# Kernel tuning notes

Hardware: AMD Instinct MI355X
Metric: run time of the kernel (lower is better)

Reference implementation:

```python
import jax, jax.numpy as jnp
import numpy as np

B, L, D, H = 4, 2048, 1024, 16
HD = D // H  # head_dim = 64


def setup_inputs() -> dict:
    key = jax.random.key(0)
    k1, k2, k3 = jax.random.split(key, 3)
    scale_in = 1.0 / np.sqrt(D)
    return {
        "x": jax.random.normal(k1, (B, L, D), dtype=jnp.float32),
        "Wqkv": jax.random.normal(k2, (D, 3 * D), dtype=jnp.float32) * scale_in,
        "Wout": jax.random.normal(k3, (D, D), dtype=jnp.float32) * scale_in,
        "bout": jnp.zeros((D,), dtype=jnp.float32),
    }


def reference(x, Wqkv, Wout, bout):
    b, l, d = x.shape
    # QKV projection (no bias): [B, L, 3D] -> [B, L, 3, H, HD]
    qkv = (x @ Wqkv).reshape(b, l, 3, H, HD)
    q, k, v = jnp.moveaxis(qkv, 2, 0)  # each [B, L, H, HD]
    # scaled scores [B, H, L, L]
    scores = jnp.einsum("blhd,bmhd->bhlm", q, k) / jnp.sqrt(jnp.float32(HD))
    causal_mask = jnp.triu(jnp.ones((l, l), dtype=bool), k=1)
    scores = jnp.where(causal_mask, -jnp.inf, scores)
    attn = jax.nn.softmax(scores, axis=-1)
    # dropout p=0.0 (eval-mode reference) -> identity
    out = jnp.einsum("bhlm,bmhd->blhd", attn, v).reshape(b, l, d)
    return out @ Wout + bout
```

## Files before the change

### kernel.cpp

```cpp
#include <hip/hip_runtime.h>

typedef unsigned short ushort_t;
using bf16x8 = __attribute__((ext_vector_type(8))) short;
using f32x4  = __attribute__((ext_vector_type(4))) float;
using f32x16 = __attribute__((ext_vector_type(16))) float;
using u32x4  = __attribute__((ext_vector_type(4))) unsigned int;

#define B_  4
#define L_  2048
#define D_  1024
#define H_  16
#define HD_ 64
#define N3_ 3072
#define M1_ (B_ * L_)

static __device__ __forceinline__ unsigned short f2bf(float f) {
    unsigned int u = __float_as_uint(f);
    unsigned int r = (u + 0x7fffu + ((u >> 16) & 1u)) >> 16;
    return (unsigned short)r;
}

static __device__ __forceinline__ unsigned int pkbf(float lo, float hi) {
    unsigned int r;
    asm("v_cvt_pk_bf16_f32 %0, %1, %2" : "=v"(r) : "v"(lo), "v"(hi));
    return r;
}

static __device__ __forceinline__ void plswap(unsigned int& a, unsigned int& b) {
    asm volatile("v_permlane32_swap_b32 %0, %1" : "+v"(a), "+v"(b));
}

static __device__ __forceinline__ void async16(const void* g, const void* l) {
    __builtin_amdgcn_global_load_lds(
        (const __attribute__((address_space(1))) void*)g,
        (__attribute__((address_space(3))) void*)l, 16, 0, 0);
}

__global__ void convert_x_kernel(const float4* __restrict__ src,
                                 ushort4* __restrict__ dst) {
    int i = blockIdx.x * blockDim.x + threadIdx.x;
    float4 v = src[i];
    ushort4 o;
    o.x = f2bf(v.x); o.y = f2bf(v.y); o.z = f2bf(v.z); o.w = f2bf(v.w);
    dst[i] = o;
}

__global__ void transpose_conv_kernel(const float* __restrict__ src,
                                      unsigned short* __restrict__ dst,
                                      int rows, int cols) {
    __shared__ float tile[32][33];
    int tx = threadIdx.x, ty = threadIdx.y;
    int c0 = blockIdx.x * 32, r0 = blockIdx.y * 32;
    #pragma unroll
    for (int j = 0; j < 32; j += 8)
        tile[ty + j][tx] = src[(size_t)(r0 + ty + j) * cols + c0 + tx];
    __syncthreads();
    #pragma unroll
    for (int j = 0; j < 32; j += 8)
        dst[(size_t)(c0 + ty + j) * rows + r0 + tx] = f2bf(tile[tx][ty + j]);
}

__global__ __launch_bounds__(512, 4) void gemm256_qkv_kernel(
    const unsigned short* __restrict__ A, const unsigned short* __restrict__ BT,
    unsigned short* __restrict__ qb, unsigned short* __restrict__ kb,
    unsigned short* __restrict__ vb) {
    constexpr int K = 1024, BK = 32, NT = K / BK;
    constexpr int NBX = N3_ / 128;
    constexpr int NWG = (M1_ / 256) * NBX;
    __shared__ __align__(16) unsigned short ldsA[3][256 * BK];
    __shared__ __align__(16) unsigned short ldsB[3][128 * BK];

    const int tid = threadIdx.x;
    const int w = tid >> 6, lane = tid & 63;
    const int wr = w >> 2, wc = w & 3;
    const int lg = lane >> 4, ll = lane & 15;

    const int bid = blockIdx.x;
    const int swz = (bid & 7) * (NWG / 8) + (bid >> 3);
    const int m0 = (swz / NBX) * 256, n0 = (swz % NBX) * 128;

    const int srow = tid >> 2;
    const int scol = (((tid & 3) ^ ((tid >> 3) & 3)) * 8);
    const int rxor = ((ll >> 1) & 3) * 8;

    f32x4 acc[8][2] = {};

    #define STAGE(kt_) do {                                                  \
        const int b3_ = (kt_) % 3;                                           \
        const size_t koff_ = (size_t)(kt_) * BK + scol;                      \
        async16(&A[(size_t)(m0 + srow) * K + koff_],       &ldsA[b3_][tid * 8]);        \
        async16(&A[(size_t)(m0 + 128 + srow) * K + koff_], &ldsA[b3_][4096 + tid * 8]); \
        async16(&BT[(size_t)(n0 + srow) * K + koff_],      &ldsB[b3_][tid * 8]);        \
    } while (0)

    STAGE(0);
    STAGE(1);

    #pragma unroll 1
    for (int kt = 0; kt < NT; ++kt) {
        if (kt + 2 < NT) {
            STAGE(kt + 2);
            asm volatile("s_waitcnt vmcnt(6)" ::: "memory");
        } else if (kt + 1 < NT) {
            asm volatile("s_waitcnt vmcnt(3)" ::: "memory");
        } else {
            asm volatile("s_waitcnt vmcnt(0)" ::: "memory");
        }
        __builtin_amdgcn_s_barrier();
        __builtin_amdgcn_sched_barrier(0);

        const unsigned short* Ab = &ldsA[kt % 3][0];
        const unsigned short* Bb = &ldsB[kt % 3][0];
        bf16x8 bfr[2];
        #pragma unroll
        for (int j = 0; j < 2; ++j)
            bfr[j] = *(const bf16x8*)&Bb[(wc * 32 + j * 16 + ll) * BK + (lg * 8 ^ rxor)];
        bf16x8 af[8];
        #pragma unroll
        for (int i = 0; i < 8; ++i)
            af[i] = *(const bf16x8*)&Ab[(wr * 128 + i * 16 + ll) * BK + (lg * 8 ^ rxor)];

        __builtin_amdgcn_s_setprio(1);
        #pragma unroll
        for (int i = 0; i < 8; ++i)
            #pragma unroll
            for (int j = 0; j < 2; ++j)
                acc[i][j] = __builtin_amdgcn_mfma_f32_16x16x32_bf16(
                    af[i], bfr[j], acc[i][j], 0, 0, 0);
        __builtin_amdgcn_s_setprio(0);
        __builtin_amdgcn_s_barrier();
    }
    #undef STAGE

    #pragma unroll
    for (int mi = 0; mi < 8; ++mi) {
        const int mb = m0 + wr * 128 + mi * 16 + lg * 4;
        #pragma unroll
        for (int ni = 0; ni < 2; ++ni) {
            const int n = n0 + wc * 32 + ni * 16 + ll;
            const int s = n >> 10, h = (n >> 6) & 15, hd = n & 63;
            if (s == 2) {
                const int b = mb >> 11, l = mb & 2047;
                const size_t base = (size_t)(b * H_ + h) * (L_ * HD_);
                ushort4 pk;
                pk.x = f2bf(acc[mi][ni][0]);
                pk.y = f2bf(acc[mi][ni][1]);
                pk.z = f2bf(acc[mi][ni][2]);
                pk.w = f2bf(acc[mi][ni][3]);
                *(ushort4*)&vb[base + (l >> 5) * 2048 + ((l >> 4) & 1) * 1024 +
                               ((l >> 3) & 1) * 512 + hd * 8 + (l & 7)] = pk;
            } else {
                #pragma unroll
                for (int r = 0; r < 4; ++r) {
                    const int m = mb + r;
                    const int b = m >> 11, l = m & 2047;
                    const size_t base = (size_t)(b * H_ + h) * (L_ * HD_);
                    const size_t o = base + (l >> 5) * 2048 + (hd >> 4) * 512 +
                                     ((hd >> 3) & 1) * 256 + (l & 31) * 8 + (hd & 7);
                    unsigned short bv = f2bf(acc[mi][ni][r]);
                    if (s == 0) qb[o] = bv; else kb[o] = bv;
                }
            }
        }
    }
}

__global__ __launch_bounds__(256) void gemm_bt_kernel(
    const unsigned short* __restrict__ A, const unsigned short* __restrict__ BT,
    float* __restrict__ outp, const float* __restrict__ bias) {
    constexpr int K = 1024;
    __shared__ unsigned short As[128 * 32];
    __shared__ unsigned short Bs[128 * 32];
    const int tid = threadIdx.x, w = tid >> 6, lane = tid & 63;
    const int m0 = blockIdx.y * 128, n0 = blockIdx.x * 128;
    const int wm = (w >> 1) * 64, wn = (w & 1) * 64;
    const int lg = lane >> 4, ll = lane & 15;
    const int scol = (((lane & 3) ^ ((lane >> 3) & 3)) * 8);
    const int rxor = ((ll >> 1) & 3) * 8;

    f32x4 acc[4][4] = {};

    for (int k0 = 0; k0 < K; k0 += 32) {
        #pragma unroll
        for (int j = 0; j < 2; ++j) {
            int row = w * 32 + j * 16 + (lane >> 2);
            async16(&A[(size_t)(m0 + row) * K + k0 + scol], &As[(w * 32 + j * 16) * 32]);
            async16(&BT[(size_t)(n0 + row) * K + k0 + scol], &Bs[(w * 32 + j * 16) * 32]);
        }
        __syncthreads();
        bf16x8 af[4], bfr[4];
        #pragma unroll
        for (int i = 0; i < 4; ++i) {
            af[i]  = *(const bf16x8*)&As[(wm + i * 16 + ll) * 32 + (lg * 8 ^ rxor)];
            bfr[i] = *(const bf16x8*)&Bs[(wn + i * 16 + ll) * 32 + (lg * 8 ^ rxor)];
        }
        #pragma unroll
        for (int mi = 0; mi < 4; ++mi)
            #pragma unroll
            for (int ni = 0; ni < 4; ++ni)
                acc[mi][ni] = __builtin_amdgcn_mfma_f32_16x16x32_bf16(
                    af[mi], bfr[ni], acc[mi][ni], 0, 0, 0);
        __syncthreads();
    }

    #pragma unroll
    for (int mi = 0; mi < 4; ++mi)
        #pragma unroll
        for (int ni = 0; ni < 4; ++ni)
            #pragma unroll
            for (int r = 0; r < 4; ++r) {
                int m = m0 + wm + mi * 16 + lg * 4 + r;
                int n = n0 + wn + ni * 16 + ll;
                outp[(size_t)m * D_ + n] = acc[mi][ni][r] + bias[n];
            }
}

__global__ __launch_bounds__(256) void attn_kernel(
    const unsigned short* __restrict__ qbuf, const unsigned short* __restrict__ kbuf,
    const unsigned short* __restrict__ vbuf, unsigned short* __restrict__ obuf) {
    __shared__ __align__(16) unsigned short ldsK[2][2048];
    __shared__ __align__(16) unsigned short ldsV[2][2048];
    __shared__ float Sden[4][32];

    const int tid = threadIdx.x;
    const int w = tid >> 6, lane = tid & 63;
    const int lq = lane & 31;
    const int hi = lane >> 5;

    const int bid = blockIdx.x;
    const int grp = bid >> 6;
    const int bh  = bid & 63;
    const int qt  = (15 - grp) * 4 + w;
    const int q0  = qt * 32;
    const int ntmax = (15 - grp) * 4 + 4;

    const unsigned short* Qf = qbuf + (size_t)bh * (L_ * HD_);
    const unsigned short* Kf = kbuf + (size_t)bh * (L_ * HD_);
    const unsigned short* Vf = vbuf + (size_t)bh * (L_ * HD_);

    bf16x8 qf[4];
    #pragma unroll
    for (int c = 0; c < 4; ++c)
        qf[c] = *(const bf16x8*)&Qf[qt * 2048 + c * 512 + hi * 256 + lq * 8];

    f32x16 oa0 = {}, oa1 = {};
    float sden = 0.f;

    const float C1 = 0.18033688011112042f;
    const float C2 = 7.2134752044448165f;

    async16(&Kf[tid * 8], &ldsK[0][tid * 8]);
    async16(&Vf[tid * 8], &ldsV[0][tid * 8]);

    #pragma unroll 1
    for (int t = 0; t < ntmax; ++t) {
        if (t + 1 < ntmax) {
            async16(&Kf[(size_t)(t + 1) * 2048 + tid * 8], &ldsK[(t + 1) & 1][tid * 8]);
            async16(&Vf[(size_t)(t + 1) * 2048 + tid * 8], &ldsV[(t + 1) & 1][tid * 8]);
            asm volatile("s_waitcnt vmcnt(2)" ::: "memory");
        } else {
            asm volatile("s_waitcnt vmcnt(0)" ::: "memory");
        }
        __builtin_amdgcn_s_barrier();
        __builtin_amdgcn_sched_barrier(0);

        if (t <= qt) {
            const unsigned short* Kb = &ldsK[t & 1][0];
            const unsigned short* Vb = &ldsV[t & 1][0];

            f32x16 st = {};
            __builtin_amdgcn_s_setprio(1);
            #pragma unroll
            for (int c = 0; c < 4; ++c) {
                bf16x8 kf = *(const bf16x8*)&Kb[c * 512 + hi * 256 + lq * 8];
                st = __builtin_amdgcn_mfma_f32_32x32x16_bf16(kf, qf[c], st, 0, 0, 0);
            }
            __builtin_amdgcn_s_setprio(0);

            float p[16];
            float rs = 0.f;
            const bool diag = (t == qt);
            #pragma unroll
            for (int r = 0; r < 16; ++r) {
                float pv = exp2f(fmaf(st[r], C1, -C2));
                if (diag) {
                    int kv = (r & 3) + 8 * (r >> 2) + 4 * hi;
                    if (kv > lq) pv = 0.f;
                }
                p[r] = pv;
                rs += pv;
            }
            rs += __shfl_xor(rs, 32);
            sden += rs;

            unsigned int a0 = pkbf(p[0],  p[1]),  a1 = pkbf(p[2],  p[3]);
            unsigned int b0 = pkbf(p[4],  p[5]),  b1 = pkbf(p[6],  p[7]);
            unsigned int c0 = pkbf(p[8],  p[9]),  c1 = pkbf(p[10], p[11]);
            unsigned int d0 = pkbf(p[12], p[13]), d1 = pkbf(p[14], p[15]);
            plswap(a0, b0);
            plswap(a1, b1);
            plswap(c0, d0);
            plswap(c1, d1);
            u32x4 t0 = {a0, a1, b0, b1};
            u32x4 t1 = {c0, c1, d0, d1};
            bf16x8 pa0 = __builtin_bit_cast(bf16x8, t0);
            bf16x8 pa1 = __builtin_bit_cast(bf16x8, t1);

            __builtin_amdgcn_s_setprio(1);
            #pragma unroll
            for (int c = 0; c < 2; ++c) {
                bf16x8 v0f = *(const bf16x8*)&Vb[c * 1024 + hi * 512 + lq * 8];
                bf16x8 v1f = *(const bf16x8*)&Vb[c * 1024 + hi * 512 + 256 + lq * 8];
                bf16x8 pa = (c == 0) ? pa0 : pa1;
                oa0 = __builtin_amdgcn_mfma_f32_32x32x16_bf16(pa, v0f, oa0, 0, 0, 0);
                oa1 = __builtin_amdgcn_mfma_f32_32x32x16_bf16(pa, v1f, oa1, 0, 0, 0);
            }
            __builtin_amdgcn_s_setprio(0);
        }
        __builtin_amdgcn_s_barrier();
    }

    if (hi == 0) Sden[w][lq] = 1.0f / sden;
    __builtin_amdgcn_s_waitcnt(0);

    const int b = bh >> 4, h = bh & 15;
    #pragma unroll
    for (int r = 0; r < 16; ++r) {
        int q = (r & 3) + 8 * (r >> 2) + 4 * hi;
        float inv = Sden[w][q];
        float o0 = oa0[r] * inv;
        float o1 = oa1[r] * inv;
        size_t row = (size_t)(b * L_ + q0 + q) * D_ + h * HD_;
        obuf[row + lq]      = f2bf(o0);
        obuf[row + 32 + lq] = f2bf(o1);
    }
}

extern "C" void kernel_launch(void* const* d_in, const int* in_sizes, int n_in,
                              void* d_out, int out_size, void* d_ws, size_t ws_size,
                              hipStream_t stream) {
    const float* x    = (const float*)d_in[0];
    const float* Wqkv = (const float*)d_in[1];
    const float* Wout = (const float*)d_in[2];
    const float* bout = (const float*)d_in[3];
    float* out = (float*)d_out;

    char* ws = (char*)d_ws;
    size_t off = 0;
    unsigned short* xb     = (unsigned short*)(ws + off); off += (size_t)M1_ * D_ * 2;
    unsigned short* wqkvT  = (unsigned short*)(ws + off); off += (size_t)N3_ * D_ * 2;
    unsigned short* woutT  = (unsigned short*)(ws + off); off += (size_t)D_ * D_ * 2;
    unsigned short* qb     = (unsigned short*)(ws + off); off += (size_t)B_ * H_ * L_ * HD_ * 2;
    unsigned short* kb     = (unsigned short*)(ws + off); off += (size_t)B_ * H_ * L_ * HD_ * 2;
    unsigned short* vb     = (unsigned short*)(ws + off); off += (size_t)B_ * H_ * L_ * HD_ * 2;
    unsigned short* attnb  = (unsigned short*)(ws + off); off += (size_t)M1_ * D_ * 2;

    convert_x_kernel<<<(M1_ * D_ / 4) / 256, 256, 0, stream>>>(
        (const float4*)x, (ushort4*)xb);
    transpose_conv_kernel<<<dim3(N3_ / 32, D_ / 32), dim3(32, 8), 0, stream>>>(
        Wqkv, wqkvT, D_, N3_);
    transpose_conv_kernel<<<dim3(D_ / 32, D_ / 32), dim3(32, 8), 0, stream>>>(
        Wout, woutT, D_, D_);

    gemm256_qkv_kernel<<<dim3((M1_ / 256) * (N3_ / 128)), 512, 0, stream>>>(
        xb, wqkvT, qb, kb, vb);

    attn_kernel<<<dim3(16 * 64), 256, 0, stream>>>(qb, kb, vb, attnb);

    gemm_bt_kernel<<<dim3(D_ / 128, M1_ / 128), 256, 0, stream>>>(
        attnb, woutT, out, bout);
}
```

Before: 199.1 us.

## Pair complementary causal query tiles per wave and load K/V directly to registers

Each wave now processes two query tiles (qt and 63-qt) so every wave does balanced causal work, sharing each K/V tile load between both. The shared-memory double buffer and block barriers are removed, and K/V fragments are read straight from global memory into registers with a one-tile K prefetch. The grid is halved to 512 blocks. This trades LDS reuse across the four waves for per-wave global loads, and raises register pressure while cutting occupancy.

```diff
diff --git a/kernel.cpp b/kernel.cpp
--- a/kernel.cpp
+++ b/kernel.cpp
@@ -218,9 +218,7 @@
 __global__ __launch_bounds__(256) void attn_kernel(
     const unsigned short* __restrict__ qbuf, const unsigned short* __restrict__ kbuf,
     const unsigned short* __restrict__ vbuf, unsigned short* __restrict__ obuf) {
-    __shared__ __align__(16) unsigned short ldsK[2][2048];
-    __shared__ __align__(16) unsigned short ldsV[2][2048];
-    __shared__ float Sden[4][32];
+    __shared__ float Sden[4][2][32];
 
     const int tid = threadIdx.x;
     const int w = tid >> 6, lane = tid & 63;
@@ -228,111 +226,156 @@
     const int hi = lane >> 5;
 
     const int bid = blockIdx.x;
-    const int grp = bid >> 6;
-    const int bh  = bid & 63;
-    const int qt  = (15 - grp) * 4 + w;
-    const int q0  = qt * 32;
-    const int ntmax = (15 - grp) * 4 + 4;
+    const int g  = bid >> 6;
+    const int bh = bid & 63;
+    const int pa = g * 4 + w;
+    const int qtA = pa, qtB = 63 - pa;
 
     const unsigned short* Qf = qbuf + (size_t)bh * (L_ * HD_);
     const unsigned short* Kf = kbuf + (size_t)bh * (L_ * HD_);
     const unsigned short* Vf = vbuf + (size_t)bh * (L_ * HD_);
 
-    bf16x8 qf[4];
-    #pragma unroll
-    for (int c = 0; c < 4; ++c)
-        qf[c] = *(const bf16x8*)&Qf[qt * 2048 + c * 512 + hi * 256 + lq * 8];
-
-    f32x16 oa0 = {}, oa1 = {};
-    float sden = 0.f;
+    bf16x8 qfA[4], qfB[4];
+    #pragma unroll
+    for (int c = 0; c < 4; ++c) {
+        qfA[c] = *(const bf16x8*)&Qf[qtA * 2048 + c * 512 + hi * 256 + lq * 8];
+        qfB[c] = *(const bf16x8*)&Qf[qtB * 2048 + c * 512 + hi * 256 + lq * 8];
+    }
+
+    f32x16 oaA0 = {}, oaA1 = {}, oaB0 = {}, oaB1 = {};
+    float sdenA = 0.f, sdenB = 0.f;
 
     const float C1 = 0.18033688011112042f;
     const float C2 = 7.2134752044448165f;
 
-    async16(&Kf[tid * 8], &ldsK[0][tid * 8]);
-    async16(&Vf[tid * 8], &ldsV[0][tid * 8]);
+    bf16x8 kf[4];
+    #pragma unroll
+    for (int c = 0; c < 4; ++c)
+        kf[c] = *(const bf16x8*)&Kf[c * 512 + hi * 256 + lq * 8];
 
     #pragma unroll 1
-    for (int t = 0; t < ntmax; ++t) {
-        if (t + 1 < ntmax) {
-            async16(&Kf[(size_t)(t + 1) * 2048 + tid * 8], &ldsK[(t + 1) & 1][tid * 8]);
-            async16(&Vf[(size_t)(t + 1) * 2048 + tid * 8], &ldsV[(t + 1) & 1][tid * 8]);
-            asm volatile("s_waitcnt vmcnt(2)" ::: "memory");
-        } else {
-            asm volatile("s_waitcnt vmcnt(0)" ::: "memory");
-        }
-        __builtin_amdgcn_s_barrier();
-        __builtin_amdgcn_sched_barrier(0);
-
-        if (t <= qt) {
-            const unsigned short* Kb = &ldsK[t & 1][0];
-            const unsigned short* Vb = &ldsV[t & 1][0];
-
-            f32x16 st = {};
-            __builtin_amdgcn_s_setprio(1);
-            #pragma unroll
-            for (int c = 0; c < 4; ++c) {
-                bf16x8 kf = *(const bf16x8*)&Kb[c * 512 + hi * 256 + lq * 8];
-                st = __builtin_amdgcn_mfma_f32_32x32x16_bf16(kf, qf[c], st, 0, 0, 0);
-            }
-            __builtin_amdgcn_s_setprio(0);
-
-            float p[16];
+    for (int t = 0; t <= qtB; ++t) {
+        bf16x8 v0f[2], v1f[2];
+        #pragma unroll
+        for (int c = 0; c < 2; ++c) {
+            v0f[c] = *(const bf16x8*)&Vf[t * 2048 + c * 1024 + hi * 512 + lq * 8];
+            v1f[c] = *(const bf16x8*)&Vf[t * 2048 + c * 1024 + hi * 512 + 256 + lq * 8];
+        }
+        bf16x8 nk[4];
+        const bool more = (t < qtB);
+        if (more) {
+            #pragma unroll
+            for (int c = 0; c < 4; ++c)
+                nk[c] = *(const bf16x8*)&Kf[(t + 1) * 2048 + c * 512 + hi * 256 + lq * 8];
+        }
+        const bool doA = (t <= qtA);
+
+        f32x16 stB = {}, stA = {};
+        __builtin_amdgcn_s_setprio(1);
+        #pragma unroll
+        for (int c = 0; c < 4; ++c)
+            stB = __builtin_amdgcn_mfma_f32_32x32x16_bf16(kf[c], qfB[c], stB, 0, 0, 0);
+        if (doA) {
+            #pragma unroll
+            for (int c = 0; c < 4; ++c)
+                stA = __builtin_amdgcn_mfma_f32_32x32x16_bf16(kf[c], qfA[c], stA, 0, 0, 0);
+        }
+        __builtin_amdgcn_s_setprio(0);
+
+        float pB[16];
+        {
             float rs = 0.f;
-            const bool diag = (t == qt);
+            const bool diag = (t == qtB);
             #pragma unroll
             for (int r = 0; r < 16; ++r) {
-                float pv = exp2f(fmaf(st[r], C1, -C2));
+                float pv = exp2f(fmaf(stB[r], C1, -C2));
                 if (diag) {
                     int kv = (r & 3) + 8 * (r >> 2) + 4 * hi;
                     if (kv > lq) pv = 0.f;
                 }
-                p[r] = pv;
+                pB[r] = pv;
                 rs += pv;
             }
             rs += __shfl_xor(rs, 32);
-            sden += rs;
-
-            unsigned int a0 = pkbf(p[0],  p[1]),  a1 = pkbf(p[2],  p[3]);
-            unsigned int b0 = pkbf(p[4],  p[5]),  b1 = pkbf(p[6],  p[7]);
-            unsigned int c0 = pkbf(p[8],  p[9]),  c1 = pkbf(p[10], p[11]);
-            unsigned int d0 = pkbf(p[12], p[13]), d1 = pkbf(p[14], p[15]);
-            plswap(a0, b0);
-            plswap(a1, b1);
-            plswap(c0, d0);
-            plswap(c1, d1);
+            sdenB += rs;
+        }
+        float pA[16];
+        if (doA) {
+            float rs = 0.f;
+            const bool diag = (t == qtA);
+            #pragma unroll
+            for (int r = 0; r < 16; ++r) {
+                float pv = exp2f(fmaf(stA[r], C1, -C2));
+                if (diag) {
+                    int kv = (r & 3) + 8 * (r >> 2) + 4 * hi;
+                    if (kv > lq) pv = 0.f;
+                }
+                pA[r] = pv;
+                rs += pv;
+            }
+            rs += __shfl_xor(rs, 32);
+            sdenA += rs;
+        }
+
+        {
+            unsigned int a0 = pkbf(pB[0],  pB[1]),  a1 = pkbf(pB[2],  pB[3]);
+            unsigned int b0 = pkbf(pB[4],  pB[5]),  b1 = pkbf(pB[6],  pB[7]);
+            unsigned int c0 = pkbf(pB[8],  pB[9]),  c1 = pkbf(pB[10], pB[11]);
+            unsigned int d0 = pkbf(pB[12], pB[13]), d1 = pkbf(pB[14], pB[15]);
+            plswap(a0, b0); plswap(a1, b1); plswap(c0, d0); plswap(c1, d1);
             u32x4 t0 = {a0, a1, b0, b1};
             u32x4 t1 = {c0, c1, d0, d1};
             bf16x8 pa0 = __builtin_bit_cast(bf16x8, t0);
             bf16x8 pa1 = __builtin_bit_cast(bf16x8, t1);
-
             __builtin_amdgcn_s_setprio(1);
-            #pragma unroll
-            for (int c = 0; c < 2; ++c) {
-                bf16x8 v0f = *(const bf16x8*)&Vb[c * 1024 + hi * 512 + lq * 8];
-                bf16x8 v1f = *(const bf16x8*)&Vb[c * 1024 + hi * 512 + 256 + lq * 8];
-                bf16x8 pa = (c == 0) ? pa0 : pa1;
-                oa0 = __builtin_amdgcn_mfma_f32_32x32x16_bf16(pa, v0f, oa0, 0, 0, 0);
-                oa1 = __builtin_amdgcn_mfma_f32_32x32x16_bf16(pa, v1f, oa1, 0, 0, 0);
-            }
+            oaB0 = __builtin_amdgcn_mfma_f32_32x32x16_bf16(pa0, v0f[0], oaB0, 0, 0, 0);
+            oaB1 = __builtin_amdgcn_mfma_f32_32x32x16_bf16(pa0, v1f[0], oaB1, 0, 0, 0);
+            oaB0 = __builtin_amdgcn_mfma_f32_32x32x16_bf16(pa1, v0f[1], oaB0, 0, 0, 0);
+            oaB1 = __builtin_amdgcn_mfma_f32_32x32x16_bf16(pa1, v1f[1], oaB1, 0, 0, 0);
             __builtin_amdgcn_s_setprio(0);
         }
-        __builtin_amdgcn_s_barrier();
-    }
-
-    if (hi == 0) Sden[w][lq] = 1.0f / sden;
+        if (doA) {
+            unsigned int a0 = pkbf(pA[0],  pA[1]),  a1 = pkbf(pA[2],  pA[3]);
+            unsigned int b0 = pkbf(pA[4],  pA[5]),  b1 = pkbf(pA[6],  pA[7]);
+            unsigned int c0 = pkbf(pA[8],  pA[9]),  c1 = pkbf(pA[10], pA[11]);
+            unsigned int d0 = pkbf(pA[12], pA[13]), d1 = pkbf(pA[14], pA[15]);
+            plswap(a0, b0); plswap(a1, b1); plswap(c0, d0); plswap(c1, d1);
+            u32x4 t0 = {a0, a1, b0, b1};
+            u32x4 t1 = {c0, c1, d0, d1};
+            bf16x8 pa0 = __builtin_bit_cast(bf16x8, t0);
+            bf16x8 pa1 = __builtin_bit_cast(bf16x8, t1);
+            __builtin_amdgcn_s_setprio(1);
+            oaA0 = __builtin_amdgcn_mfma_f32_32x32x16_bf16(pa0, v0f[0], oaA0, 0, 0, 0);
+            oaA1 = __builtin_amdgcn_mfma_f32_32x32x16_bf16(pa0, v1f[0], oaA1, 0, 0, 0);
+            oaA0 = __builtin_amdgcn_mfma_f32_32x32x16_bf16(pa1, v0f[1], oaA0, 0, 0, 0);
+            oaA1 = __builtin_amdgcn_mfma_f32_32x32x16_bf16(pa1, v1f[1], oaA1, 0, 0, 0);
+            __builtin_amdgcn_s_setprio(0);
+        }
+
+        if (more) {
+            #pragma unroll
+            for (int c = 0; c < 4; ++c) kf[c] = nk[c];
+        }
+    }
+
+    if (hi == 0) {
+        Sden[w][0][lq] = 1.0f / sdenA;
+        Sden[w][1][lq] = 1.0f / sdenB;
+    }
     __builtin_amdgcn_s_waitcnt(0);
 
     const int b = bh >> 4, h = bh & 15;
     #pragma unroll
     for (int r = 0; r < 16; ++r) {
         int q = (r & 3) + 8 * (r >> 2) + 4 * hi;
-        float inv = Sden[w][q];
-        float o0 = oa0[r] * inv;
-        float o1 = oa1[r] * inv;
-        size_t row = (size_t)(b * L_ + q0 + q) * D_ + h * HD_;
-        obuf[row + lq]      = f2bf(o0);
-        obuf[row + 32 + lq] = f2bf(o1);
+        float invA = Sden[w][0][q];
+        float invB = Sden[w][1][q];
+        size_t rowA = (size_t)(b * L_ + qtA * 32 + q) * D_ + h * HD_;
+        size_t rowB = (size_t)(b * L_ + qtB * 32 + q) * D_ + h * HD_;
+        obuf[rowA + lq]      = f2bf(oaA0[r] * invA);
+        obuf[rowA + 32 + lq] = f2bf(oaA1[r] * invA);
+        obuf[rowB + lq]      = f2bf(oaB0[r] * invB);
+        obuf[rowB + 32 + lq] = f2bf(oaB1[r] * invB);
     }
 }
 
@@ -365,7 +408,7 @@
     gemm256_qkv_kernel<<<dim3((M1_ / 256) * (N3_ / 128)), 512, 0, stream>>>(
         xb, wqkvT, qb, kb, vb);
 
-    attn_kernel<<<dim3(16 * 64), 256, 0, stream>>>(qb, kb, vb, attnb);
+    attn_kernel<<<dim3(8 * 64), 256, 0, stream>>>(qb, kb, vb, attnb);
 
     gemm_bt_kernel<<<dim3(D_ / 128, M1_ / 128), 256, 0, stream>>>(
         attnb, woutT, out, bout);
```

New measurement: 231.7 us. +16.4%, slower.
